# Kernel tuning notes

Hardware: AMD Instinct MI355X
Metric: run time of the kernel (lower is better)

The kernel has to match this reference:

```python
import jax, jax.numpy as jnp
import numpy as np

N_NODES = 100000
N_EDGES = 1600000
F_IN = 128
HIDDEN = 128
N_CLASSES = 32
N_GRAPHS = 64


def setup_inputs() -> dict:
    key = jax.random.key(0)
    ks = jax.random.split(key, 10)
    x = jax.random.normal(ks[0], (N_NODES, F_IN), dtype=jnp.float32)
    edge_index = jax.random.randint(ks[1], (2, N_EDGES), 0, N_NODES, dtype=jnp.int64)
    batch = jnp.sort(jax.random.randint(ks[2], (N_NODES,), 0, N_GRAPHS, dtype=jnp.int64))
    s1 = 1.0 / np.sqrt(F_IN)
    s2 = 1.0 / np.sqrt(HIDDEN)
    W1 = jax.random.normal(ks[3], (F_IN, HIDDEN), dtype=jnp.float32) * s1
    b1 = jnp.zeros((HIDDEN,), dtype=jnp.float32)
    W2 = jax.random.normal(ks[4], (HIDDEN, HIDDEN), dtype=jnp.float32) * s2
    b2 = jnp.zeros((HIDDEN,), dtype=jnp.float32)
    fcW = jax.random.normal(ks[5], (HIDDEN, N_CLASSES), dtype=jnp.float32) * s2
    fcb = jnp.zeros((N_CLASSES,), dtype=jnp.float32)
    return {"x": x, "edge_index": edge_index, "batch": batch,
            "W1": W1, "b1": b1, "W2": W2, "b2": b2, "fcW": fcW, "fcb": fcb}


def _gcn_layer(x, src, dst, W, b, num_nodes):
    # PyG GCNConv: h = X W; out = D^-1/2 (A + I) D^-1/2 h + b,
    # degrees computed over incoming edges at dst, including self-loops.
    h = x @ W  # [N, H]
    ones = jnp.ones(src.shape[0], dtype=x.dtype)
    deg = jax.ops.segment_sum(ones, dst, num_segments=num_nodes) + 1.0  # +1 self-loop
    dinv = jax.lax.rsqrt(deg)  # [N]
    enorm = dinv[src] * dinv[dst]  # [E] per-edge symmetric normalization
    agg = jax.ops.segment_sum(h[src] * enorm[:, None], dst, num_segments=num_nodes)
    agg = agg + h * (dinv * dinv)[:, None]  # self-loop message
    return agg + b


def reference(x, edge_index, batch, W1, b1, W2, b2, fcW, fcb):
    num_nodes = x.shape[0]
    src, dst = edge_index[0], edge_index[1]
    h = jax.nn.relu(_gcn_layer(x, src, dst, W1, b1, num_nodes))
    h = jax.nn.relu(_gcn_layer(h, src, dst, W2, b2, num_nodes))
    # global mean pool per graph
    sums = jax.ops.segment_sum(h, batch, num_segments=N_GRAPHS)  # [G, H]
    cnt = jax.ops.segment_sum(jnp.ones((num_nodes, 1), h.dtype), batch, num_segments=N_GRAPHS)
    pooled = sums / jnp.maximum(cnt, 1.0)
    return pooled @ fcW + fcb  # [G, C]
```

## Files before the change

kernel.cpp:

```cpp
#include <hip/hip_runtime.h>
#include <hip/hip_bf16.h>

#define N_NODES   100000
#define FDIM      128
#define N_GRAPHS  64
#define N_CLASSES 32

#define NB        ((N_NODES + 255) / 256)
#define EPB       8192
#define SCAN_CHUNK 2048

typedef __attribute__((ext_vector_type(8))) short short8;
typedef __attribute__((ext_vector_type(4))) float f32x4;

__device__ __forceinline__ float bf2f(unsigned int u16) {
    unsigned int x = u16 << 16;
    return __builtin_bit_cast(float, x);
}
__device__ __forceinline__ unsigned short f2bf(float f) {
    unsigned int u = __builtin_bit_cast(unsigned int, f);
    unsigned int r = (u + 0x7fffu + ((u >> 16) & 1u)) >> 16;
    return (unsigned short)r;
}

__global__ __launch_bounds__(256) void hist_kernel(const int* __restrict__ dst, int* __restrict__ hist,
                                                   int nE, int nblk) {
    __shared__ int h[NB];
    int t = threadIdx.x, blk = blockIdx.x;
    for (int i = t; i < NB; i += 256) h[i] = 0;
    __syncthreads();
    int base = blk * EPB;
    #pragma unroll
    for (int j = 0; j < EPB / 256; ++j) {
        int e = base + j * 256 + t;
        if (e < nE) atomicAdd(&h[dst[e] >> 8], 1);
    }
    __syncthreads();
    for (int i = t; i < NB; i += 256) hist[i * nblk + blk] = h[i];
}

__global__ __launch_bounds__(256) void scan_p1(const int* __restrict__ a, int* __restrict__ bsums, int n) {
    __shared__ int wsum[4];
    int b = blockIdx.x, t = threadIdx.x;
    int base = b * SCAN_CHUNK;
    int sum = 0;
    #pragma unroll
    for (int j = 0; j < SCAN_CHUNK / 256; ++j) {
        int idx = base + j * 256 + t;
        sum += (idx < n) ? a[idx] : 0;
    }
    #pragma unroll
    for (int off = 32; off; off >>= 1) sum += __shfl_down(sum, off, 64);
    int lane = t & 63, w = t >> 6;
    if (lane == 0) wsum[w] = sum;
    __syncthreads();
    if (t == 0) bsums[b] = wsum[0] + wsum[1] + wsum[2] + wsum[3];
}

__global__ __launch_bounds__(64) void scan_p2(int* __restrict__ bsums, int nb) {
    int t = threadIdx.x;
    int carry = 0;
    for (int base = 0; base < nb; base += 64) {
        int i = base + t;
        int v = (i < nb) ? bsums[i] : 0;
        int inc = v;
        #pragma unroll
        for (int off = 1; off < 64; off <<= 1) {
            int y = __shfl_up(inc, off, 64);
            if (t >= off) inc += y;
        }
        if (i < nb) bsums[i] = carry + inc - v;
        carry += __shfl(inc, 63, 64);
    }
}

__global__ __launch_bounds__(256) void scan_p3(const int* __restrict__ a, const int* __restrict__ bsums,
                                               int* __restrict__ out, int n) {
    __shared__ int wsum[4];
    int b = blockIdx.x, t = threadIdx.x;
    int lane = t & 63, w = t >> 6;
    int i0 = b * SCAN_CHUNK + t * 8;
    int v[8];
    int s = 0;
    #pragma unroll
    for (int j = 0; j < 8; ++j) {
        int idx = i0 + j;
        v[j] = (idx < n) ? a[idx] : 0;
        s += v[j];
    }
    int ps = s;
    #pragma unroll
    for (int off = 1; off < 64; off <<= 1) {
        int y = __shfl_up(ps, off, 64);
        if (lane >= off) ps += y;
    }
    if (lane == 63) wsum[w] = ps;
    __syncthreads();
    if (t == 0) {
        int acc = 0;
        #pragma unroll
        for (int i = 0; i < 4; ++i) { int tmp = wsum[i]; wsum[i] = acc; acc += tmp; }
    }
    __syncthreads();
    int run = (ps - s) + wsum[w] + bsums[b];
    #pragma unroll
    for (int j = 0; j < 8; ++j) {
        int idx = i0 + j;
        if (idx < n) out[idx] = run;
        run += v[j];
    }
}

__global__ __launch_bounds__(256) void part_kernel(const int* __restrict__ src, const int* __restrict__ dst,
                                                   const int* __restrict__ offs,
                                                   unsigned long long* __restrict__ recs,
                                                   int nE, int nblk) {
    __shared__ int cur[NB];
    int t = threadIdx.x, blk = blockIdx.x;
    for (int i = t; i < NB; i += 256) cur[i] = offs[i * nblk + blk];
    __syncthreads();
    int base = blk * EPB;
    #pragma unroll
    for (int j = 0; j < EPB / 256; ++j) {
        int e = base + j * 256 + t;
        if (e < nE) {
            int s = src[e], d = dst[e];
            int pos = atomicAdd(&cur[d >> 8], 1);
            recs[pos] = (unsigned long long)(unsigned)s | ((unsigned long long)(unsigned)d << 32);
        }
    }
}

__global__ __launch_bounds__(256) void csr_kernel(const unsigned long long* __restrict__ recs,
                                                  const int* __restrict__ offs,
                                                  int* __restrict__ row_ptr, int* __restrict__ esrc,
                                                  float* __restrict__ dinv, int nE, int nblk) {
    __shared__ int cnt[256];
    __shared__ int cur[256];
    __shared__ int wsum[4];
    int b = blockIdx.x, t = threadIdx.x;
    int node0 = b << 8;
    int segBeg = offs[b * nblk];
    int segEnd = (b + 1 < NB) ? offs[(b + 1) * nblk] : nE;
    cnt[t] = 0;
    __syncthreads();
    for (int e = segBeg + t; e < segEnd; e += 256) {
        int d = (int)(recs[e] >> 32);
        atomicAdd(&cnt[d - node0], 1);
    }
    __syncthreads();
    int c = cnt[t];
    int lane = t & 63, w = t >> 6;
    int ps = c;
    #pragma unroll
    for (int off = 1; off < 64; off <<= 1) {
        int y = __shfl_up(ps, off, 64);
        if (lane >= off) ps += y;
    }
    if (lane == 63) wsum[w] = ps;
    __syncthreads();
    if (t == 0) {
        int a = 0;
        #pragma unroll
        for (int i = 0; i < 4; ++i) { int tmp = wsum[i]; wsum[i] = a; a += tmp; }
    }
    __syncthreads();
    int gbase = segBeg + (ps - c) + wsum[w];
    cur[t] = gbase;
    int node = node0 + t;
    if (node < N_NODES) {
        row_ptr[node] = gbase;
        dinv[node] = rsqrtf((float)c + 1.0f);
    }
    if (b == NB - 1 && t == 0) row_ptr[N_NODES] = nE;
    __syncthreads();
    for (int e = segBeg + t; e < segEnd; e += 256) {
        unsigned long long r = recs[e];
        int d = (int)(r >> 32);
        int pos = atomicAdd(&cur[d - node0], 1);
        esrc[pos] = (int)(r & 0xffffffffu);
    }
}

__global__ __launch_bounds__(256) void wtrans(const float* __restrict__ W, unsigned short* __restrict__ WT) {
    int idx = blockIdx.x * 256 + threadIdx.x;
    int k = idx >> 7, n = idx & 127;
    WT[n * 128 + k] = f2bf(W[idx]);
}

template<int IN_F32>
__global__ __launch_bounds__(256) void gemm_mfma(const void* __restrict__ Xv,
                                                 const unsigned short* __restrict__ WT,
                                                 unsigned short* __restrict__ H, int nrows) {
    __shared__ char lds[65536];
    char* xs  = lds;
    char* wsh = lds + 32768;
    int t = threadIdx.x;
    int base = blockIdx.x * 128;

    #pragma unroll
    for (int j = 0; j < 8; ++j) {
        int idx = j * 256 + t;
        int n = idx >> 4, c8 = idx & 15;
        short8 v = *(const short8*)(WT + n * 128 + c8 * 8);
        int off = (n * 256 + c8 * 16) ^ ((n & 7) << 4);
        *(short8*)(wsh + off) = v;
    }
    #pragma unroll
    for (int j = 0; j < 8; ++j) {
        int idx = j * 256 + t;
        int row = idx >> 4, c8 = idx & 15;
        int grow = base + row;
        short8 v = {0,0,0,0,0,0,0,0};
        if (grow < nrows) {
            if (IN_F32) {
                const float* Xf = (const float*)Xv;
                float4 a = *(const float4*)(Xf + (size_t)grow * 128 + c8 * 8);
                float4 b = *(const float4*)(Xf + (size_t)grow * 128 + c8 * 8 + 4);
                v[0] = (short)f2bf(a.x); v[1] = (short)f2bf(a.y);
                v[2] = (short)f2bf(a.z); v[3] = (short)f2bf(a.w);
                v[4] = (short)f2bf(b.x); v[5] = (short)f2bf(b.y);
                v[6] = (short)f2bf(b.z); v[7] = (short)f2bf(b.w);
            } else {
                const unsigned short* Xb = (const unsigned short*)Xv;
                v = *(const short8*)(Xb + (size_t)grow * 128 + c8 * 8);
            }
        }
        int off = (row * 256 + c8 * 16) ^ ((row & 7) << 4);
        *(short8*)(xs + off) = v;
    }
    __syncthreads();

    int lane = t & 63, w = t >> 6;
    int lhi = lane >> 4, llo = lane & 15;
    f32x4 acc[2][8];
    #pragma unroll
    for (int r = 0; r < 2; ++r)
        #pragma unroll
        for (int c = 0; c < 8; ++c) acc[r][c] = (f32x4){0.f, 0.f, 0.f, 0.f};

    #pragma unroll
    for (int kk = 0; kk < 4; ++kk) {
        short8 a[2];
        #pragma unroll
        for (int r = 0; r < 2; ++r) {
            int row = w * 32 + r * 16 + llo;
            int off = (row * 256 + kk * 64 + lhi * 16) ^ ((row & 7) << 4);
            a[r] = *(const short8*)(xs + off);
        }
        #pragma unroll
        for (int c = 0; c < 8; ++c) {
            int col = c * 16 + llo;
            int off = (col * 256 + kk * 64 + lhi * 16) ^ ((col & 7) << 4);
            short8 bb = *(const short8*)(wsh + off);
            acc[0][c] = __builtin_amdgcn_mfma_f32_16x16x32_bf16(a[0], bb, acc[0][c], 0, 0, 0);
            acc[1][c] = __builtin_amdgcn_mfma_f32_16x16x32_bf16(a[1], bb, acc[1][c], 0, 0, 0);
        }
    }

    #pragma unroll
    for (int r = 0; r < 2; ++r) {
        #pragma unroll
        for (int reg = 0; reg < 4; ++reg) {
            int grow = base + w * 32 + r * 16 + lhi * 4 + reg;
            if (grow < nrows) {
                #pragma unroll
                for (int c = 0; c < 8; ++c)
                    H[(size_t)grow * 128 + c * 16 + llo] = f2bf(acc[r][c][reg]);
            }
        }
    }
}

__global__ __launch_bounds__(256) void agg_bf16(const unsigned short* __restrict__ H,
                                                unsigned short* __restrict__ O,
                                                const float* __restrict__ dinv,
                                                const int* __restrict__ row_ptr,
                                                const int* __restrict__ esrc,
                                                const float* __restrict__ bias) {
    int node = blockIdx.x * 4 + (threadIdx.x >> 6);
    if (node >= N_NODES) return;
    int lane = threadIdx.x & 63;
    int g  = lane >> 4;
    int fl = lane & 15;

    float dv = dinv[node];
    float acc[8];
    {
        short8 hv = *(const short8*)(H + (size_t)node * FDIM + fl * 8);
        float sw = (g == 0) ? dv * dv : 0.f;
        #pragma unroll
        for (int j = 0; j < 8; ++j) acc[j] = bf2f((unsigned short)hv[j]) * sw;
    }

    int beg = row_ptr[node], end = row_ptr[node + 1];
    for (int e0 = beg; e0 < end; e0 += 16) {
        int eb = e0 + g * 4;
        int s[4];
        float wg[4];
        #pragma unroll
        for (int u = 0; u < 4; ++u) {
            int e = eb + u;
            int ee = min(e, end - 1);
            s[u] = esrc[ee];
            wg[u] = (e < end) ? dinv[s[u]] * dv : 0.f;
        }
        #pragma unroll
        for (int u = 0; u < 4; ++u) {
            short8 m = *(const short8*)(H + (size_t)s[u] * FDIM + fl * 8);
            float wgt = wg[u];
            #pragma unroll
            for (int j = 0; j < 8; ++j) acc[j] += bf2f((unsigned short)m[j]) * wgt;
        }
    }

    #pragma unroll
    for (int j = 0; j < 8; ++j) {
        acc[j] += __shfl_xor(acc[j], 16, 64);
        acc[j] += __shfl_xor(acc[j], 32, 64);
    }

    float4 b0 = *(const float4*)(bias + fl * 8);
    float4 b1 = *(const float4*)(bias + fl * 8 + 4);
    float r0 = fmaxf(acc[0] + b0.x, 0.f), r1 = fmaxf(acc[1] + b0.y, 0.f);
    float r2 = fmaxf(acc[2] + b0.z, 0.f), r3 = fmaxf(acc[3] + b0.w, 0.f);
    float r4 = fmaxf(acc[4] + b1.x, 0.f), r5 = fmaxf(acc[5] + b1.y, 0.f);
    float r6 = fmaxf(acc[6] + b1.z, 0.f), r7 = fmaxf(acc[7] + b1.w, 0.f);
    if (g == 0) {
        short8 v;
        v[0] = (short)f2bf(r0); v[1] = (short)f2bf(r1);
        v[2] = (short)f2bf(r2); v[3] = (short)f2bf(r3);
        v[4] = (short)f2bf(r4); v[5] = (short)f2bf(r5);
        v[6] = (short)f2bf(r6); v[7] = (short)f2bf(r7);
        *(short8*)(O + (size_t)node * FDIM + fl * 8) = v;
    }
}

__global__ __launch_bounds__(128) void pool_kernel(const unsigned short* __restrict__ H, const int* __restrict__ batch,
                                                   float* __restrict__ pooled, float* __restrict__ cnt) {
    int f  = threadIdx.x;
    int r0 = blockIdx.x * 128;
    int rend = r0 + 128; if (rend > N_NODES) rend = N_NODES;
    if (r0 >= N_NODES) return;
    float acc = 0.f;
    int g_cur = batch[r0];
    int run = 0;
    for (int r = r0; r < rend; ++r) {
        int g = batch[r];
        if (g != g_cur) {
            atomicAdd(&pooled[g_cur * FDIM + f], acc);
            if (f == 0) atomicAdd(&cnt[g_cur], (float)run);
            acc = 0.f; run = 0; g_cur = g;
        }
        acc += bf2f(H[(size_t)r * FDIM + f]);
        run++;
    }
    atomicAdd(&pooled[g_cur * FDIM + f], acc);
    if (f == 0) atomicAdd(&cnt[g_cur], (float)run);
}

__global__ __launch_bounds__(256) void fc_kernel(const float* __restrict__ pooled, const float* __restrict__ cnt,
                                                 const float* __restrict__ fcW, const float* __restrict__ fcb,
                                                 float* __restrict__ out) {
    int idx = blockIdx.x * 256 + threadIdx.x;
    if (idx >= N_GRAPHS * N_CLASSES) return;
    int g = idx >> 5, c = idx & 31;
    float inv = 1.0f / fmaxf(cnt[g], 1.0f);
    float acc = 0.f;
    #pragma unroll 16
    for (int k = 0; k < FDIM; ++k) acc += pooled[g * FDIM + k] * fcW[k * N_CLASSES + c];
    out[idx] = acc * inv + fcb[c];
}

extern "C" void kernel_launch(void* const* d_in, const int* in_sizes, int n_in,
                              void* d_out, int out_size, void* d_ws, size_t ws_size,
                              hipStream_t stream) {
    const float* x    = (const float*)d_in[0];
    const int*   ei   = (const int*)d_in[1];
    const int*   batch= (const int*)d_in[2];
    const float* W1   = (const float*)d_in[3];
    const float* b1   = (const float*)d_in[4];
    const float* W2   = (const float*)d_in[5];
    const float* b2   = (const float*)d_in[6];
    const float* fcW  = (const float*)d_in[7];
    const float* fcb  = (const float*)d_in[8];
    float* out = (float*)d_out;

    const int nE = in_sizes[1] / 2;
    const int* src = ei;
    const int* dst = ei + nE;

    const int nblk  = (nE + EPB - 1) / EPB;
    const int histN = NB * nblk;
    const int sB    = (histN + SCAN_CHUNK - 1) / SCAN_CHUNK;

    unsigned short* Hb0 = (unsigned short*)d_ws;
    unsigned short* Hb1 = Hb0 + (size_t)N_NODES * FDIM;
    unsigned short* W1T = Hb1 + (size_t)N_NODES * FDIM;
    unsigned short* W2T = W1T + FDIM * FDIM;
    float* dinv    = (float*)(W2T + FDIM * FDIM);
    int*   row_ptr = (int*)(dinv + N_NODES);
    int*   esrc    = row_ptr + N_NODES + 1;
    unsigned long long* recs = (unsigned long long*)(esrc + ((nE + 1) & ~1));
    int*   hist    = (int*)(recs + nE);
    int*   bsums   = hist + histN;
    float* pooled  = (float*)(bsums + ((sB + 1) & ~1));
    float* cnt     = pooled + N_GRAPHS * FDIM;

    hipMemsetAsync(pooled, 0, (N_GRAPHS * FDIM + N_GRAPHS) * sizeof(float), stream);

    wtrans<<<64, 256, 0, stream>>>(W1, W1T);
    wtrans<<<64, 256, 0, stream>>>(W2, W2T);

    hist_kernel<<<nblk, 256, 0, stream>>>(dst, hist, nE, nblk);
    scan_p1<<<sB, 256, 0, stream>>>(hist, bsums, histN);
    scan_p2<<<1, 64, 0, stream>>>(bsums, sB);
    scan_p3<<<sB, 256, 0, stream>>>(hist, bsums, hist, histN);
    part_kernel<<<nblk, 256, 0, stream>>>(src, dst, hist, recs, nE, nblk);
    csr_kernel<<<NB, 256, 0, stream>>>(recs, hist, row_ptr, esrc, dinv, nE, nblk);

    const int gemm_grid = (N_NODES + 127) / 128;
    gemm_mfma<1><<<gemm_grid, 256, 0, stream>>>(x, W1T, Hb0, N_NODES);
    agg_bf16<<<(N_NODES + 3) / 4, 256, 0, stream>>>(Hb0, Hb1, dinv, row_ptr, esrc, b1);
    gemm_mfma<0><<<gemm_grid, 256, 0, stream>>>(Hb1, W2T, Hb0, N_NODES);
    agg_bf16<<<(N_NODES + 3) / 4, 256, 0, stream>>>(Hb0, Hb1, dinv, row_ptr, esrc, b2);

    pool_kernel<<<(N_NODES + 127) / 128, 128, 0, stream>>>(Hb1, batch, pooled, cnt);
    fc_kernel<<<(N_GRAPHS * N_CLASSES + 255) / 256, 256, 0, stream>>>(pooled, cnt, fcW, fcb, out);
}
```

Before: 400.0 us.

## Fold self-loops into CSR, cache edge weights, stage GEMM stores through LDS

The CSR build now inserts each node's self-loop as an explicit edge, so the aggregation no longer does a separate self-row load. The first aggregation layer writes per-edge normalization weights to a buffer that the second layer reads back, which removes the dependent dinv[src] gather. The GEMM epilogue stages bf16 results in LDS and writes full 16-byte rows instead of scattered 2-byte stores. The two weight-transpose launches are merged into one. In exchange this adds an extra weight buffer and its memory traffic, plus a more complex workspace layout.

Result: faster. 385.5 us (-3.6%).

```diff
diff --git a/kernel.cpp b/kernel.cpp
--- a/kernel.cpp
+++ b/kernel.cpp
@@ -165,14 +165,17 @@
         for (int i = 0; i < 4; ++i) { int tmp = wsum[i]; wsum[i] = a; a += tmp; }
     }
     __syncthreads();
-    int gbase = segBeg + (ps - c) + wsum[w];
-    cur[t] = gbase;
     int node = node0 + t;
+    int rbase = segBeg + node0 + (ps - c) + wsum[w] + t;
     if (node < N_NODES) {
-        row_ptr[node] = gbase;
+        row_ptr[node] = rbase;
+        esrc[rbase] = node;
         dinv[node] = rsqrtf((float)c + 1.0f);
-    }
-    if (b == NB - 1 && t == 0) row_ptr[N_NODES] = nE;
+        cur[t] = rbase + 1;
+    } else {
+        cur[t] = 0;
+    }
+    if (b == NB - 1 && t == 0) row_ptr[N_NODES] = nE + N_NODES;
     __syncthreads();
     for (int e = segBeg + t; e < segEnd; e += 256) {
         unsigned long long r = recs[e];
@@ -182,10 +185,14 @@
     }
 }
 
-__global__ __launch_bounds__(256) void wtrans(const float* __restrict__ W, unsigned short* __restrict__ WT) {
+__global__ __launch_bounds__(256) void wtrans2(const float* __restrict__ W1, const float* __restrict__ W2,
+                                               unsigned short* __restrict__ W1T, unsigned short* __restrict__ W2T) {
     int idx = blockIdx.x * 256 + threadIdx.x;
-    int k = idx >> 7, n = idx & 127;
-    WT[n * 128 + k] = f2bf(W[idx]);
+    const float* W = (idx < 16384) ? W1 : W2;
+    unsigned short* WT = (idx < 16384) ? W1T : W2T;
+    int i = idx & 16383;
+    int k = i >> 7, n = i & 127;
+    WT[n * 128 + k] = f2bf(W[i]);
 }
 
 template<int IN_F32>
@@ -258,25 +265,35 @@
         }
     }
 
+    __syncthreads();
+    unsigned short* ct = (unsigned short*)lds;
     #pragma unroll
     for (int r = 0; r < 2; ++r) {
         #pragma unroll
         for (int reg = 0; reg < 4; ++reg) {
-            int grow = base + w * 32 + r * 16 + lhi * 4 + reg;
-            if (grow < nrows) {
-                #pragma unroll
-                for (int c = 0; c < 8; ++c)
-                    H[(size_t)grow * 128 + c * 16 + llo] = f2bf(acc[r][c][reg]);
-            }
-        }
-    }
-}
-
+            int row = w * 32 + r * 16 + lhi * 4 + reg;
+            #pragma unroll
+            for (int c = 0; c < 8; ++c)
+                ct[row * 128 + c * 16 + llo] = f2bf(acc[r][c][reg]);
+        }
+    }
+    __syncthreads();
+    #pragma unroll
+    for (int k = 0; k < 8; ++k) {
+        int elem = w * 4096 + k * 512 + lane * 8;
+        int row = elem >> 7, col = elem & 127;
+        if (base + row < nrows)
+            *(short8*)(H + (size_t)(base + row) * 128 + col) = *(const short8*)(ct + elem);
+    }
+}
+
+template<int LAYER>
 __global__ __launch_bounds__(256) void agg_bf16(const unsigned short* __restrict__ H,
                                                 unsigned short* __restrict__ O,
                                                 const float* __restrict__ dinv,
                                                 const int* __restrict__ row_ptr,
                                                 const int* __restrict__ esrc,
+                                                float* __restrict__ wbuf,
                                                 const float* __restrict__ bias) {
     int node = blockIdx.x * 4 + (threadIdx.x >> 6);
     if (node >= N_NODES) return;
@@ -286,12 +303,8 @@
 
     float dv = dinv[node];
     float acc[8];
-    {
-        short8 hv = *(const short8*)(H + (size_t)node * FDIM + fl * 8);
-        float sw = (g == 0) ? dv * dv : 0.f;
-        #pragma unroll
-        for (int j = 0; j < 8; ++j) acc[j] = bf2f((unsigned short)hv[j]) * sw;
-    }
+    #pragma unroll
+    for (int j = 0; j < 8; ++j) acc[j] = 0.f;
 
     int beg = row_ptr[node], end = row_ptr[node + 1];
     for (int e0 = beg; e0 < end; e0 += 16) {
@@ -303,7 +316,14 @@
             int e = eb + u;
             int ee = min(e, end - 1);
             s[u] = esrc[ee];
-            wg[u] = (e < end) ? dinv[s[u]] * dv : 0.f;
+            bool val = e < end;
+            if (LAYER == 0) {
+                float wv = dinv[s[u]] * dv;
+                wg[u] = val ? wv : 0.f;
+                if (val && fl == 0) wbuf[e] = wv;
+            } else {
+                wg[u] = val ? wbuf[ee] : 0.f;
+            }
         }
         #pragma unroll
         for (int u = 0; u < 4; ++u) {
@@ -393,6 +413,7 @@
     const int nblk  = (nE + EPB - 1) / EPB;
     const int histN = NB * nblk;
     const int sB    = (histN + SCAN_CHUNK - 1) / SCAN_CHUNK;
+    const int nSlots = nE + N_NODES;
 
     unsigned short* Hb0 = (unsigned short*)d_ws;
     unsigned short* Hb1 = Hb0 + (size_t)N_NODES * FDIM;
@@ -401,7 +422,9 @@
     float* dinv    = (float*)(W2T + FDIM * FDIM);
     int*   row_ptr = (int*)(dinv + N_NODES);
     int*   esrc    = row_ptr + N_NODES + 1;
-    unsigned long long* recs = (unsigned long long*)(esrc + ((nE + 1) & ~1));
+    float* wbuf    = (float*)(esrc + nSlots);
+    unsigned long long* recs = (unsigned long long*)
+        ((char*)(wbuf + nSlots) + (((size_t)(wbuf + nSlots)) & 4 ? 4 : 0));
     int*   hist    = (int*)(recs + nE);
     int*   bsums   = hist + histN;
     float* pooled  = (float*)(bsums + ((sB + 1) & ~1));
@@ -409,8 +432,7 @@
 
     hipMemsetAsync(pooled, 0, (N_GRAPHS * FDIM + N_GRAPHS) * sizeof(float), stream);
 
-    wtrans<<<64, 256, 0, stream>>>(W1, W1T);
-    wtrans<<<64, 256, 0, stream>>>(W2, W2T);
+    wtrans2<<<128, 256, 0, stream>>>(W1, W2, W1T, W2T);
 
     hist_kernel<<<nblk, 256, 0, stream>>>(dst, hist, nE, nblk);
     scan_p1<<<sB, 256, 0, stream>>>(hist, bsums, histN);
@@ -421,9 +443,9 @@
 
     const int gemm_grid = (N_NODES + 127) / 128;
     gemm_mfma<1><<<gemm_grid, 256, 0, stream>>>(x, W1T, Hb0, N_NODES);
-    agg_bf16<<<(N_NODES + 3) / 4, 256, 0, stream>>>(Hb0, Hb1, dinv, row_ptr, esrc, b1);
+    agg_bf16<0><<<(N_NODES + 3) / 4, 256, 0, stream>>>(Hb0, Hb1, dinv, row_ptr, esrc, wbuf, b1);
     gemm_mfma<0><<<gemm_grid, 256, 0, stream>>>(Hb1, W2T, Hb0, N_NODES);
-    agg_bf16<<<(N_NODES + 3) / 4, 256, 0, stream>>>(Hb0, Hb1, dinv, row_ptr, esrc, b2);
+    agg_bf16<1><<<(N_NODES + 3) / 4, 256, 0, stream>>>(Hb0, Hb1, dinv, row_ptr, esrc, wbuf, b2);
 
     pool_kernel<<<(N_NODES + 127) / 128, 128, 0, stream>>>(Hb1, batch, pooled, cnt);
     fc_kernel<<<(N_GRAPHS * N_CLASSES + 255) / 256, 256, 0, stream>>>(pooled, cnt, fcW, fcb, out);
```

## Sort CSR neighbor lists, merge weight transposes, stage GEMM output through LDS

Applied to the files above, without the earlier changes.

Three unrelated changes land together. After CSR construction, each node's source list is insertion-sorted so the gather in aggregation visits rows in increasing address order, which may improve cache locality. The two weight-transpose kernels become one launch. The GEMM epilogue now writes results into LDS first and then stores them as coalesced 16-byte vectors instead of scattered 2-byte stores, at the cost of an extra barrier and LDS round trip.

Result: slower. 497.8 us (+24.4%).

```diff
diff --git a/kernel.cpp b/kernel.cpp
--- a/kernel.cpp
+++ b/kernel.cpp
@@ -180,12 +180,26 @@
         int pos = atomicAdd(&cur[d - node0], 1);
         esrc[pos] = (int)(r & 0xffffffffu);
     }
-}
-
-__global__ __launch_bounds__(256) void wtrans(const float* __restrict__ W, unsigned short* __restrict__ WT) {
+    __syncthreads();
+    if (node < N_NODES && c > 1) {
+        int lo = gbase, hi = gbase + c;
+        for (int i = lo + 1; i < hi; ++i) {
+            int key = esrc[i];
+            int j = i - 1;
+            while (j >= lo && esrc[j] > key) { esrc[j + 1] = esrc[j]; --j; }
+            esrc[j + 1] = key;
+        }
+    }
+}
+
+__global__ __launch_bounds__(256) void wtrans2(const float* __restrict__ W1, const float* __restrict__ W2,
+                                               unsigned short* __restrict__ W1T, unsigned short* __restrict__ W2T) {
     int idx = blockIdx.x * 256 + threadIdx.x;
-    int k = idx >> 7, n = idx & 127;
-    WT[n * 128 + k] = f2bf(W[idx]);
+    const float* W = (idx < 16384) ? W1 : W2;
+    unsigned short* WT = (idx < 16384) ? W1T : W2T;
+    int i = idx & 16383;
+    int k = i >> 7, n = i & 127;
+    WT[n * 128 + k] = f2bf(W[i]);
 }
 
 template<int IN_F32>
@@ -258,17 +272,25 @@
         }
     }
 
+    __syncthreads();
+    unsigned short* ct = (unsigned short*)lds;
     #pragma unroll
     for (int r = 0; r < 2; ++r) {
         #pragma unroll
         for (int reg = 0; reg < 4; ++reg) {
-            int grow = base + w * 32 + r * 16 + lhi * 4 + reg;
-            if (grow < nrows) {
-                #pragma unroll
-                for (int c = 0; c < 8; ++c)
-                    H[(size_t)grow * 128 + c * 16 + llo] = f2bf(acc[r][c][reg]);
-            }
-        }
+            int row = w * 32 + r * 16 + lhi * 4 + reg;
+            #pragma unroll
+            for (int c = 0; c < 8; ++c)
+                ct[row * 128 + c * 16 + llo] = f2bf(acc[r][c][reg]);
+        }
+    }
+    __syncthreads();
+    #pragma unroll
+    for (int k = 0; k < 8; ++k) {
+        int elem = w * 4096 + k * 512 + lane * 8;
+        int row = elem >> 7, col = elem & 127;
+        if (base + row < nrows)
+            *(short8*)(H + (size_t)(base + row) * 128 + col) = *(const short8*)(ct + elem);
     }
 }
 
@@ -409,8 +431,7 @@
 
     hipMemsetAsync(pooled, 0, (N_GRAPHS * FDIM + N_GRAPHS) * sizeof(float), stream);
 
-    wtrans<<<64, 256, 0, stream>>>(W1, W1T);
-    wtrans<<<64, 256, 0, stream>>>(W2, W2T);
+    wtrans2<<<128, 256, 0, stream>>>(W1, W2, W1T, W2T);
 
     hist_kernel<<<nblk, 256, 0, stream>>>(dst, hist, nE, nblk);
     scan_p1<<<sB, 256, 0, stream>>>(hist, bsums, histN);
```
